# Optimization experiments

Hardware: AMD Instinct MI355X
Metric: run time of the kernel (lower is better)

## Reference

```python
import jax, jax.numpy as jnp
import numpy as np

B, C, H, T = 20, 395, 10, 8192  # batch, input channels, hidden, seq len
GATE_IN = 2 * C + H             # = 800, matches Linear(800, 10)
INIT_IN = 87                    # initilaizer = Linear(87, hidden)


def _uni(k, shape, fan_in):
    s = 1.0 / np.sqrt(fan_in)
    return jax.random.uniform(k, shape, jnp.float32, -s, s)


def setup_inputs() -> dict:
    key = jax.random.key(0)
    ks = jax.random.split(key, 12)
    x = jax.random.normal(ks[0], (B, C, T), jnp.float32)
    y = jax.random.normal(ks[1], (B, C, T), jnp.float32)
    Wf = _uni(ks[2], (H, GATE_IN), GATE_IN); bf = _uni(ks[3], (H,), GATE_IN)
    Wi = _uni(ks[4], (H, GATE_IN), GATE_IN); bi = _uni(ks[5], (H,), GATE_IN)
    Wu = _uni(ks[6], (H, GATE_IN), GATE_IN); bu = _uni(ks[7], (H,), GATE_IN)
    Wo = _uni(ks[8], (H, GATE_IN), GATE_IN); bo = _uni(ks[9], (H,), GATE_IN)
    W_init = _uni(ks[10], (H, INIT_IN), INIT_IN); b_init = _uni(ks[11], (H,), INIT_IN)
    return dict(x=x, y=y, Wf=Wf, bf=bf, Wi=Wi, bi=bi, Wu=Wu, bu=bu,
                Wo=Wo, bo=bo, W_init=W_init, b_init=b_init)


def reference(x, y, Wf, bf, Wi, bi, Wu, bu, Wo, bo, W_init, b_init):
    b_, c_, t_ = x.shape
    h_ = Wf.shape[0]
    # initial states: h0 zeros; c0 = Linear(87->H)(zeros(20,87)) == broadcast bias
    h0 = jnp.zeros((b_, h_), x.dtype)
    c0 = jnp.zeros((b_, INIT_IN), x.dtype) @ W_init.T + b_init  # (B, H)
    # y_prev[t] = y[t-1], zeros at t=0
    y_prev = jnp.concatenate([jnp.zeros((b_, c_, 1), x.dtype), y[..., :-1]], axis=-1)
    # stacked input per step is [x_t, h, y_prev]; split weights accordingly
    W = jnp.stack([Wf, Wi, Wu, Wo])           # (4, H, 2C+H)
    bvec = jnp.stack([bf, bi, bu, bo])        # (4, H)
    Wx, Wh, Wy = W[..., :c_], W[..., c_:c_ + h_], W[..., c_ + h_:]
    # precompute all input-dependent gate pre-activations: (T, B, 4, H)
    pre = (jnp.einsum('bct,ghc->tbgh', x, Wx)
           + jnp.einsum('bct,ghc->tbgh', y_prev, Wy)
           + bvec)

    def step(carry, pre_t):
        h, c = carry
        z = pre_t + jnp.einsum('bh,goh->bgo', h, Wh)  # (B, 4, H)
        f = jax.nn.sigmoid(z[:, 0])
        i = jax.nn.sigmoid(z[:, 1])
        g = jnp.tanh(z[:, 2])
        o = jax.nn.sigmoid(z[:, 3])
        c = c * f + i * g
        h = o * jnp.tanh(c)
        return (h, c), h

    (_, cT), hs = jax.lax.scan(step, (h0, c0), pre)  # hs: (T, B, H)
    out = jnp.moveaxis(hs, 0, -1)  # (B, H, T), matches torch.stack(..., dim=-1)
    return out, cT
```

## Files before the change

kernel.cpp:

```cpp
#include <hip/hip_runtime.h>

#define Bn 20
#define Cn 395
#define Hn 10
#define Tn 8192
#define TP (Tn + 8)
#define GIN 800
#define CP 400
#define NL2E (-1.4426950408889634f)

__global__ __launch_bounds__(256) void pclstm_wt(
    const float* __restrict__ Wf, const float* __restrict__ Wi,
    const float* __restrict__ Wu, const float* __restrict__ Wo,
    float* __restrict__ wt)
{
  int i = blockIdx.x * 256 + threadIdx.x;
  if (i >= CP * 80) return;
  int c = i / 80;
  int q = i - c * 80;
  float v = 0.f;
  if (c < Cn) {
    int qq = (q < 40) ? q : q - 40;
    int h = qq >> 2;
    int g = qq & 3;
    const float* W = (g == 0) ? Wf : (g == 1) ? Wi : (g == 2) ? Wu : Wo;
    float s = (g == 2) ? 2.f * NL2E : NL2E;
    int col = (q < 40) ? c : (Cn + Hn + c);
    v = W[h * GIN + col] * s;
  }
  wt[i] = v;
}

#define SC 80
#define NSTAGE (CP / SC)

__global__ __launch_bounds__(256) void pclstm_pre(
    const float* __restrict__ x, const float* __restrict__ y,
    const float* __restrict__ wt, float* __restrict__ pre)
{
  __shared__ float4 wls[SC * 20];

  const int tid = threadIdx.x;
  const int b = blockIdx.y;
  const int t0 = blockIdx.x * 512 + tid;
  const int t1 = t0 + 256;

  const float* xb0 = x + (size_t)b * Cn * Tn + t0;
  const float* xb1 = xb0 + 256;
  const float* yb0 = y + (size_t)b * Cn * Tn + ((t0 > 0) ? t0 - 1 : 0);
  const float* yb1 = y + (size_t)b * Cn * Tn + (t1 - 1);
  const float ym0 = (t0 > 0) ? 1.f : 0.f;

  float acc0[40], acc1[40];
#pragma unroll
  for (int q = 0; q < 40; ++q) { acc0[q] = 0.f; acc1[q] = 0.f; }

  float xr0[8], yr0[8], xr1[8], yr1[8];
#pragma unroll
  for (int d = 0; d < 8; ++d) {
    xr0[d] = xb0[(size_t)d * Tn];
    yr0[d] = ym0 * yb0[(size_t)d * Tn];
    xr1[d] = xb1[(size_t)d * Tn];
    yr1[d] = yb1[(size_t)d * Tn];
  }

  const float4* wt4 = reinterpret_cast<const float4*>(wt);

  for (int s = 0; s < NSTAGE; ++s) {
    __syncthreads();
#pragma unroll
    for (int i = 0; i < 7; ++i) {
      int idx = i * 256 + tid;
      if (idx < SC * 20) wls[idx] = wt4[(size_t)s * (SC * 20) + idx];
    }
    __syncthreads();

#pragma unroll 8
    for (int cc = 0; cc < SC; ++cc) {
      const int c = s * SC + cc;
      const int slot = cc & 7;
      float xv0 = xr0[slot], yv0 = yr0[slot];
      float xv1 = xr1[slot], yv1 = yr1[slot];
      int cp = c + 8;
      cp = (cp < Cn) ? cp : (Cn - 1);
      xr0[slot] = xb0[(size_t)cp * Tn];
      yr0[slot] = ym0 * yb0[(size_t)cp * Tn];
      xr1[slot] = xb1[(size_t)cp * Tn];
      yr1[slot] = yb1[(size_t)cp * Tn];

      const float4* wr4 = &wls[cc * 20];
#pragma unroll
      for (int k = 0; k < 10; ++k) {
        float4 wx = wr4[k];
        float4 wy = wr4[k + 10];
        acc0[4*k+0] = fmaf(xv0, wx.x, acc0[4*k+0]);
        acc0[4*k+1] = fmaf(xv0, wx.y, acc0[4*k+1]);
        acc0[4*k+2] = fmaf(xv0, wx.z, acc0[4*k+2]);
        acc0[4*k+3] = fmaf(xv0, wx.w, acc0[4*k+3]);
        acc1[4*k+0] = fmaf(xv1, wx.x, acc1[4*k+0]);
        acc1[4*k+1] = fmaf(xv1, wx.y, acc1[4*k+1]);
        acc1[4*k+2] = fmaf(xv1, wx.z, acc1[4*k+2]);
        acc1[4*k+3] = fmaf(xv1, wx.w, acc1[4*k+3]);
        acc0[4*k+0] = fmaf(yv0, wy.x, acc0[4*k+0]);
        acc0[4*k+1] = fmaf(yv0, wy.y, acc0[4*k+1]);
        acc0[4*k+2] = fmaf(yv0, wy.z, acc0[4*k+2]);
        acc0[4*k+3] = fmaf(yv0, wy.w, acc0[4*k+3]);
        acc1[4*k+0] = fmaf(yv1, wy.x, acc1[4*k+0]);
        acc1[4*k+1] = fmaf(yv1, wy.y, acc1[4*k+1]);
        acc1[4*k+2] = fmaf(yv1, wy.z, acc1[4*k+2]);
        acc1[4*k+3] = fmaf(yv1, wy.w, acc1[4*k+3]);
      }
    }
  }

  float4* dst0 = reinterpret_cast<float4*>(pre + ((size_t)b * TP + t0) * 40);
  float4* dst1 = reinterpret_cast<float4*>(pre + ((size_t)b * TP + t1) * 40);
#pragma unroll
  for (int k = 0; k < 10; ++k) {
    float4 v4;
    v4.x = acc0[4*k+0]; v4.y = acc0[4*k+1]; v4.z = acc0[4*k+2]; v4.w = acc0[4*k+3];
    dst0[k] = v4;
    float4 w4;
    w4.x = acc1[4*k+0]; w4.y = acc1[4*k+1]; w4.z = acc1[4*k+2]; w4.w = acc1[4*k+3];
    dst1[k] = w4;
  }
}

#define QP(v, ctrl) __int_as_float(__builtin_amdgcn_update_dpp( \
    0, __float_as_int(v), (ctrl), 0xf, 0xf, true))

__global__ __launch_bounds__(64) void pclstm_scan(
    const float* __restrict__ pre,
    const float* __restrict__ Wf, const float* __restrict__ Wi,
    const float* __restrict__ Wu, const float* __restrict__ Wo,
    const float* __restrict__ bfp, const float* __restrict__ bip,
    const float* __restrict__ bup, const float* __restrict__ bop,
    const float* __restrict__ b_init,
    float* __restrict__ out)
{
  const int b = blockIdx.x;
  const int l = threadIdx.x;
  const int lc = (l < 40) ? l : 39;
  const int o = lc >> 2;
  const int g = lc & 3;

  const float* W  = (g == 0) ? Wf : (g == 1) ? Wi : (g == 2) ? Wu : Wo;
  const float* bp = (g == 0) ? bfp : (g == 1) ? bip : (g == 2) ? bup : bop;
  const float sg  = (g == 2) ? 2.f * NL2E : NL2E;
  const float ag  = (g == 2) ? 2.f : 1.f;
  const float bgc = (g == 2) ? -1.f : 0.f;

  float wh[10];
#pragma unroll
  for (int j = 0; j < 10; ++j) wh[j] = W[o * GIN + Cn + j] * sg;
  const float sgb = sg * bp[o];

  const float* preb = pre + (size_t)b * TP * 40 + lc;
  float c = b_init[o];
  float h = 0.f;
  float hb[10];
#pragma unroll
  for (int j = 0; j < 10; ++j) hb[j] = 0.f;

  float pbuf[8];
#pragma unroll
  for (int k = 0; k < 8; ++k) pbuf[k] = preb[(size_t)k * 40];

  const bool sl = (l < 40) && (g == 3);
  float* outb = out + (size_t)b * Hn * Tn;
  float hs[4];

#pragma unroll 8
  for (int t = 0; t < Tn; ++t) {
    float pv = pbuf[t & 7];
    pbuf[t & 7] = preb[(size_t)(t + 8) * 40];

    float pvs = pv + sgb;

    float m1 = wh[2] * hb[2];
    float m2 = wh[4] * hb[4];
    float m3 = wh[6] * hb[6];
    float m4 = wh[8] * hb[8];
    float s0 = fmaf(wh[0], hb[0], pvs);
    float s1 = fmaf(wh[1], hb[1], m1);
    float s2 = fmaf(wh[3], hb[3], m2);
    float s3 = fmaf(wh[5], hb[5], m3);
    float s4 = fmaf(wh[7], hb[7], m4);
    s0 = fmaf(wh[9], hb[9], s0);
    float zs = (s0 + s1) + (s2 + (s3 + s4));

    float e = __builtin_amdgcn_exp2f(zs);
    float r = __builtin_amdgcn_rcpf(1.f + e);
    float gate = fmaf(ag, r, bgc);

    float fv = QP(gate, 0x00);
    float iv = QP(gate, 0x55);
    float uv = QP(gate, 0xAA);
    float ov = QP(gate, 0xFF);

    c = fmaf(c, fv, iv * uv);
    float zc = (2.f * NL2E) * c;
    float e2 = __builtin_amdgcn_exp2f(zc);
    float r2 = __builtin_amdgcn_rcpf(1.f + e2);
    float th = fmaf(2.f, r2, -1.f);
    h = ov * th;

    hs[t & 3] = h;
    if (((t & 3) == 3) && sl) {
      float4 v4; v4.x = hs[0]; v4.y = hs[1]; v4.z = hs[2]; v4.w = hs[3];
      *reinterpret_cast<float4*>(outb + (size_t)o * Tn + t - 3) = v4;
    }

#pragma unroll
    for (int j = 0; j < 10; ++j)
      hb[j] = __int_as_float(__builtin_amdgcn_readlane(__float_as_int(h), 4 * j));
  }
  if ((l < 40) && (g == 0)) out[(size_t)Bn * Hn * Tn + b * Hn + o] = c;
}

extern "C" void kernel_launch(void* const* d_in, const int* in_sizes, int n_in,
                              void* d_out, int out_size, void* d_ws, size_t ws_size,
                              hipStream_t stream) {
  const float* x      = (const float*)d_in[0];
  const float* y      = (const float*)d_in[1];
  const float* Wf     = (const float*)d_in[2];
  const float* bf     = (const float*)d_in[3];
  const float* Wi     = (const float*)d_in[4];
  const float* bi     = (const float*)d_in[5];
  const float* Wu     = (const float*)d_in[6];
  const float* bu     = (const float*)d_in[7];
  const float* Wo     = (const float*)d_in[8];
  const float* bo     = (const float*)d_in[9];
  const float* b_init = (const float*)d_in[11];
  float* out = (float*)d_out;

  float* wt  = (float*)d_ws;
  float* pre = (float*)((char*)d_ws + 131072);

  pclstm_wt<<<(CP * 80 + 255) / 256, 256, 0, stream>>>(Wf, Wi, Wu, Wo, wt);
  dim3 g1(Tn / 512, Bn);
  pclstm_pre<<<g1, 256, 0, stream>>>(x, y, wt, pre);
  pclstm_scan<<<Bn, 64, 0, stream>>>(pre, Wf, Wi, Wu, Wo, bf, bi, bu, bo, b_init, out);
}
```

Before: 1.463 ms.

## Split channel reduction across two blocks and rescale scan cell state

The precompute kernel now splits the 400-channel reduction into two halves along a new grid dimension. Each half writes its own partial pre-activation buffer, which doubles the block count (16x20 to 16x20x2) to fill more CUs, and launch bounds request three blocks per CU. The scan kernel sums the two partial buffers per step, keeps the cell state pre-scaled by the exp2 constant to drop a multiply from the serial chain, and folds the tanh affine into one fma with the output gate. It also writes outputs in 8-element chunks. The cost is twice the pre-activation writes and reads, plus an extra add and load per step in the latency-bound scan.

```diff
diff --git a/kernel.cpp b/kernel.cpp
--- a/kernel.cpp
+++ b/kernel.cpp
@@ -8,6 +8,7 @@
 #define GIN 800
 #define CP 400
 #define NL2E (-1.4426950408889634f)
+#define KC (2.f * NL2E)
 
 __global__ __launch_bounds__(256) void pclstm_wt(
     const float* __restrict__ Wf, const float* __restrict__ Wi,
@@ -31,17 +32,21 @@
   wt[i] = v;
 }
 
-#define SC 80
-#define NSTAGE (CP / SC)
-
-__global__ __launch_bounds__(256) void pclstm_pre(
+#define SC 40
+#define CHALF 200
+#define NST (CHALF / SC)
+
+__global__ __launch_bounds__(256, 3) void pclstm_pre(
     const float* __restrict__ x, const float* __restrict__ y,
-    const float* __restrict__ wt, float* __restrict__ pre)
+    const float* __restrict__ wt,
+    float* __restrict__ preA, float* __restrict__ preB)
 {
   __shared__ float4 wls[SC * 20];
 
   const int tid = threadIdx.x;
   const int b = blockIdx.y;
+  const int ch = blockIdx.z;
+  const int c0 = ch * CHALF;
   const int t0 = blockIdx.x * 512 + tid;
   const int t1 = t0 + 256;
 
@@ -58,26 +63,26 @@
   float xr0[8], yr0[8], xr1[8], yr1[8];
 #pragma unroll
   for (int d = 0; d < 8; ++d) {
-    xr0[d] = xb0[(size_t)d * Tn];
-    yr0[d] = ym0 * yb0[(size_t)d * Tn];
-    xr1[d] = xb1[(size_t)d * Tn];
-    yr1[d] = yb1[(size_t)d * Tn];
+    xr0[d] = xb0[(size_t)(c0 + d) * Tn];
+    yr0[d] = ym0 * yb0[(size_t)(c0 + d) * Tn];
+    xr1[d] = xb1[(size_t)(c0 + d) * Tn];
+    yr1[d] = yb1[(size_t)(c0 + d) * Tn];
   }
 
   const float4* wt4 = reinterpret_cast<const float4*>(wt);
 
-  for (int s = 0; s < NSTAGE; ++s) {
+  for (int s = 0; s < NST; ++s) {
     __syncthreads();
 #pragma unroll
-    for (int i = 0; i < 7; ++i) {
+    for (int i = 0; i < 4; ++i) {
       int idx = i * 256 + tid;
-      if (idx < SC * 20) wls[idx] = wt4[(size_t)s * (SC * 20) + idx];
+      if (idx < SC * 20) wls[idx] = wt4[(size_t)(c0 + s * SC) * 20 + idx];
     }
     __syncthreads();
 
 #pragma unroll 8
     for (int cc = 0; cc < SC; ++cc) {
-      const int c = s * SC + cc;
+      const int c = c0 + s * SC + cc;
       const int slot = cc & 7;
       float xv0 = xr0[slot], yv0 = yr0[slot];
       float xv1 = xr1[slot], yv1 = yr1[slot];
@@ -113,8 +118,9 @@
     }
   }
 
-  float4* dst0 = reinterpret_cast<float4*>(pre + ((size_t)b * TP + t0) * 40);
-  float4* dst1 = reinterpret_cast<float4*>(pre + ((size_t)b * TP + t1) * 40);
+  float* dsthalf = (ch == 0) ? preA : preB;
+  float4* dst0 = reinterpret_cast<float4*>(dsthalf + ((size_t)b * TP + t0) * 40);
+  float4* dst1 = reinterpret_cast<float4*>(dsthalf + ((size_t)b * TP + t1) * 40);
 #pragma unroll
   for (int k = 0; k < 10; ++k) {
     float4 v4;
@@ -130,7 +136,7 @@
     0, __float_as_int(v), (ctrl), 0xf, 0xf, true))
 
 __global__ __launch_bounds__(64) void pclstm_scan(
-    const float* __restrict__ pre,
+    const float* __restrict__ preA, const float* __restrict__ preB,
     const float* __restrict__ Wf, const float* __restrict__ Wi,
     const float* __restrict__ Wu, const float* __restrict__ Wo,
     const float* __restrict__ bfp, const float* __restrict__ bip,
@@ -140,48 +146,51 @@
 {
   const int b = blockIdx.x;
   const int l = threadIdx.x;
-  const int lc = (l < 40) ? l : 39;
-  const int o = lc >> 2;
-  const int g = lc & 3;
+  if (l >= 40) return;
+  const int o = l >> 2;
+  const int g = l & 3;
 
   const float* W  = (g == 0) ? Wf : (g == 1) ? Wi : (g == 2) ? Wu : Wo;
   const float* bp = (g == 0) ? bfp : (g == 1) ? bip : (g == 2) ? bup : bop;
   const float sg  = (g == 2) ? 2.f * NL2E : NL2E;
-  const float ag  = (g == 2) ? 2.f : 1.f;
-  const float bgc = (g == 2) ? -1.f : 0.f;
+  const float ag  = (g == 2) ? 2.f * KC : 1.f;
+  const float bgc = (g == 2) ? -KC : 0.f;
 
   float wh[10];
 #pragma unroll
   for (int j = 0; j < 10; ++j) wh[j] = W[o * GIN + Cn + j] * sg;
   const float sgb = sg * bp[o];
 
-  const float* preb = pre + (size_t)b * TP * 40 + lc;
-  float c = b_init[o];
+  const float* prebA = preA + (size_t)b * TP * 40 + l;
+  const float* prebB = preB + (size_t)b * TP * 40 + l;
+  float cs = KC * b_init[o];
   float h = 0.f;
   float hb[10];
 #pragma unroll
   for (int j = 0; j < 10; ++j) hb[j] = 0.f;
 
-  float pbuf[8];
-#pragma unroll
-  for (int k = 0; k < 8; ++k) pbuf[k] = preb[(size_t)k * 40];
-
-  const bool sl = (l < 40) && (g == 3);
+  float pbA[8], pbB[8];
+#pragma unroll
+  for (int k = 0; k < 8; ++k) {
+    pbA[k] = prebA[(size_t)k * 40];
+    pbB[k] = prebB[(size_t)k * 40];
+  }
+
+  const bool sl = (g == 3);
   float* outb = out + (size_t)b * Hn * Tn;
-  float hs[4];
+  float hs[8];
 
 #pragma unroll 8
   for (int t = 0; t < Tn; ++t) {
-    float pv = pbuf[t & 7];
-    pbuf[t & 7] = preb[(size_t)(t + 8) * 40];
-
-    float pvs = pv + sgb;
+    float pv = (pbA[t & 7] + pbB[t & 7]) + sgb;
+    pbA[t & 7] = prebA[(size_t)(t + 8) * 40];
+    pbB[t & 7] = prebB[(size_t)(t + 8) * 40];
 
     float m1 = wh[2] * hb[2];
     float m2 = wh[4] * hb[4];
     float m3 = wh[6] * hb[6];
     float m4 = wh[8] * hb[8];
-    float s0 = fmaf(wh[0], hb[0], pvs);
+    float s0 = fmaf(wh[0], hb[0], pv);
     float s1 = fmaf(wh[1], hb[1], m1);
     float s2 = fmaf(wh[3], hb[3], m2);
     float s3 = fmaf(wh[5], hb[5], m3);
@@ -198,24 +207,27 @@
     float uv = QP(gate, 0xAA);
     float ov = QP(gate, 0xFF);
 
-    c = fmaf(c, fv, iv * uv);
-    float zc = (2.f * NL2E) * c;
-    float e2 = __builtin_amdgcn_exp2f(zc);
+    float ov2 = ov + ov;
+    float ovn = -ov;
+    cs = fmaf(cs, fv, iv * uv);
+    float e2 = __builtin_amdgcn_exp2f(cs);
     float r2 = __builtin_amdgcn_rcpf(1.f + e2);
-    float th = fmaf(2.f, r2, -1.f);
-    h = ov * th;
-
-    hs[t & 3] = h;
-    if (((t & 3) == 3) && sl) {
+    h = fmaf(ov2, r2, ovn);
+
+    hs[t & 7] = h;
+    if (((t & 7) == 7) && sl) {
       float4 v4; v4.x = hs[0]; v4.y = hs[1]; v4.z = hs[2]; v4.w = hs[3];
-      *reinterpret_cast<float4*>(outb + (size_t)o * Tn + t - 3) = v4;
+      float4 w4; w4.x = hs[4]; w4.y = hs[5]; w4.z = hs[6]; w4.w = hs[7];
+      float* p = outb + (size_t)o * Tn + t - 7;
+      *reinterpret_cast<float4*>(p) = v4;
+      *reinterpret_cast<float4*>(p + 4) = w4;
     }
 
 #pragma unroll
     for (int j = 0; j < 10; ++j)
       hb[j] = __int_as_float(__builtin_amdgcn_readlane(__float_as_int(h), 4 * j));
   }
-  if ((l < 40) && (g == 0)) out[(size_t)Bn * Hn * Tn + b * Hn + o] = c;
+  if (g == 0) out[(size_t)Bn * Hn * Tn + b * Hn + o] = cs * (1.f / KC);
 }
 
 extern "C" void kernel_launch(void* const* d_in, const int* in_sizes, int n_in,
@@ -234,11 +246,13 @@
   const float* b_init = (const float*)d_in[11];
   float* out = (float*)d_out;
 
-  float* wt  = (float*)d_ws;
-  float* pre = (float*)((char*)d_ws + 131072);
+  const size_t PRE_B = (size_t)Bn * TP * 40 * 4;
+  float* wt   = (float*)d_ws;
+  float* preA = (float*)((char*)d_ws + 131072);
+  float* preB = (float*)((char*)d_ws + 131072 + PRE_B);
 
   pclstm_wt<<<(CP * 80 + 255) / 256, 256, 0, stream>>>(Wf, Wi, Wu, Wo, wt);
-  dim3 g1(Tn / 512, Bn);
-  pclstm_pre<<<g1, 256, 0, stream>>>(x, y, wt, pre);
-  pclstm_scan<<<Bn, 64, 0, stream>>>(pre, Wf, Wi, Wu, Wo, bf, bi, bu, bo, b_init, out);
-}
+  dim3 g1(Tn / 512, Bn, 2);
+  pclstm_pre<<<g1, 256, 0, stream>>>(x, y, wt, preA, preB);
+  pclstm_scan<<<Bn, 64, 0, stream>>>(preA, preB, Wf, Wi, Wu, Wo, bf, bi, bu, bo, b_init, out);
+}
```

After: 1.593 ms. +8.9%, slower.
